# Kernel tuning notes

Measured on AMD Instinct MI355X. Metric: run time of the kernel, lower is better.

Reference implementation:

```python
import jax, jax.numpy as jnp
import numpy as np

N_EXPERTS = 8
D_IN = 1024
D_OUT = 1024
BATCH = 4096


def setup_inputs() -> dict:
    key = jax.random.key(0)
    k_x, k_w, k_b, k_a = jax.random.split(key, 4)
    xs = jax.random.normal(k_x, (BATCH, D_IN), dtype=jnp.float32)
    mxs = jnp.arange(BATCH, dtype=jnp.int32)  # opaque per-sample metadata, passed through
    actions = jax.random.randint(k_a, (BATCH,), 0, N_EXPERTS, dtype=jnp.int64)
    # Expert parameters: each submodule is Linear(D_IN -> D_OUT)
    W = jax.random.normal(k_w, (N_EXPERTS, D_OUT, D_IN), dtype=jnp.float32) / np.sqrt(D_IN)
    b = jax.random.normal(k_b, (N_EXPERTS, D_OUT), dtype=jnp.float32) * 0.01
    return {"xs": xs, "mxs": mxs, "actions": actions, "W": W, "b": b}


def reference(xs, mxs, actions, W, b):
    # Original: per-sample python loop y_i = submodule[actions[i]](x_i); cat along batch.
    # Vectorized: compute all experts densely (E small), then select per-sample row.
    y_all = jnp.einsum("bj,eij->bei", xs, W) + b[None, :, :]  # [B, E, D_OUT]
    ys = jnp.take_along_axis(y_all, actions[:, None, None].astype(jnp.int32), axis=1)
    ys = jnp.squeeze(ys, axis=1)  # [B, D_OUT]
    return (ys, mxs, actions)
```

## Files before the change

kernel.cpp:

```cpp
#include <hip/hip_runtime.h>

#define BATCH 4096
#define D_IN 1024
#define D_OUT 1024
#define N_EXPERTS 8

#define TM 64
#define TN 128
#define TK 32
#define MAX_TILES 71

#define WS_PERM    0
#define WS_STARTS  4096
#define WS_TILE_E  4112
#define WS_TILE_M  4200
#define WS_NTILES  4288

typedef __attribute__((ext_vector_type(8))) short short8;
typedef __attribute__((ext_vector_type(4))) float f32x4;

__global__ void group_kernel(const int* __restrict__ actions, int* __restrict__ ws) {
    __shared__ int cnt[N_EXPERTS];
    __shared__ int base[N_EXPERTS];
    const int t = threadIdx.x;
    if (t < N_EXPERTS) cnt[t] = 0;
    __syncthreads();
    for (int i = t; i < BATCH; i += 256) atomicAdd(&cnt[actions[i]], 1);
    __syncthreads();
    if (t == 0) {
        int s = 0, nt = 0;
        for (int e = 0; e < N_EXPERTS; ++e) {
            const int c = cnt[e];
            base[e] = s;
            ws[WS_STARTS + e] = s;
            for (int m0 = 0; m0 < c; m0 += TM) {
                ws[WS_TILE_E + nt] = e;
                ws[WS_TILE_M + nt] = m0;
                ++nt;
            }
            s += c;
            cnt[e] = 0;
        }
        ws[WS_STARTS + N_EXPERTS] = s;
        ws[WS_NTILES] = nt;
    }
    __syncthreads();
    for (int i = t; i < BATCH; i += 256) {
        const int a = actions[i];
        const int pos = base[a] + atomicAdd(&cnt[a], 1);
        ws[WS_PERM + pos] = i;
    }
}

__device__ __forceinline__ void cvt8(const float4 a, const float4 b,
                                     short8& h, short8& l) {
    float f[8] = {a.x, a.y, a.z, a.w, b.x, b.y, b.z, b.w};
#pragma unroll
    for (int i = 0; i < 8; ++i) {
        const unsigned u = __float_as_uint(f[i]);
        h[i] = (short)(u >> 16);
        const float r = f[i] - __uint_as_float(u & 0xffff0000u);
        l[i] = (short)(__float_as_uint(r) >> 16);
    }
}

__global__ __launch_bounds__(256) void moe_gemm(
    const float* __restrict__ xs, const float* __restrict__ W,
    const float* __restrict__ bias, const int* __restrict__ ws,
    float* __restrict__ out)
{
    const int tix = blockIdx.y;
    if (tix >= ws[WS_NTILES]) return;
    const int e   = ws[WS_TILE_E + tix];
    const int m0  = ws[WS_TILE_M + tix];
    const int s0  = ws[WS_STARTS + e];
    const int cnt = ws[WS_STARTS + e + 1] - s0;
    const int n0  = blockIdx.x * TN;

    __shared__ short Ahi[TM * TK];
    __shared__ short Alo[TM * TK];
    __shared__ short Bhi[TN * TK];
    __shared__ short Blo[TN * TK];
    __shared__ int   rows_s[TM];

    const int t = threadIdx.x;
    if (t < TM) {
        const int r = m0 + t;
        rows_s[t] = (r < cnt) ? ws[WS_PERM + s0 + r] : -1;
    }
    __syncthreads();

    const int lane = t & 63;
    const int wave = t >> 6;
    const int wm = (wave & 1) * 32;
    const int wn = (wave >> 1) * 64;

    const float zf = 0.f;
    f32x4 acc[2][4];
#pragma unroll
    for (int mi = 0; mi < 2; ++mi)
#pragma unroll
        for (int nj = 0; nj < 4; ++nj)
            acc[mi][nj] = (f32x4){zf, zf, zf, zf};

    const float* Wb = W + (size_t)e * (D_OUT * (size_t)D_IN) + (size_t)n0 * D_IN;

    const int j  = t & 3;
    const int rr = t >> 2;

    const int arow = rows_s[rr];
    const float* aptr = (arow >= 0) ? (xs + (size_t)arow * D_IN + j * 8) : nullptr;

    const int slotA   = (j * 16 + (rr & 15)) ^ (j << 1);
    const int aoff_st = (rr >> 4) * 512 + slotA * 8;
    const int boff0   = aoff_st;
    const int boff1   = aoff_st + 4 * 512;

    const float* qb0 = Wb + (size_t)rr * D_IN + j * 8;
    const float* qb1 = Wb + (size_t)(64 + rr) * D_IN + j * 8;

    const int rds = (lane ^ ((lane >> 4) << 1)) * 8;

    float4 ra0 = make_float4(0.f, 0.f, 0.f, 0.f), ra1 = ra0;
    if (aptr) { ra0 = *(const float4*)(aptr);     ra1 = *(const float4*)(aptr + 4); }
    float4 rb0 = *(const float4*)(qb0),           rb1 = *(const float4*)(qb0 + 4);
    float4 rb2 = *(const float4*)(qb1),           rb3 = *(const float4*)(qb1 + 4);

    for (int k0 = 0; ; ) {
        {
            short8 h, l;
            cvt8(ra0, ra1, h, l);
            *(short8*)&Ahi[aoff_st] = h;
            *(short8*)&Alo[aoff_st] = l;
            cvt8(rb0, rb1, h, l);
            *(short8*)&Bhi[boff0] = h;
            *(short8*)&Blo[boff0] = l;
            cvt8(rb2, rb3, h, l);
            *(short8*)&Bhi[boff1] = h;
            *(short8*)&Blo[boff1] = l;
        }
        __syncthreads();

        const int kn = k0 + TK;
        if (kn < D_IN) {
            if (aptr) {
                ra0 = *(const float4*)(aptr + kn);
                ra1 = *(const float4*)(aptr + kn + 4);
            }
            rb0 = *(const float4*)(qb0 + kn); rb1 = *(const float4*)(qb0 + kn + 4);
            rb2 = *(const float4*)(qb1 + kn); rb3 = *(const float4*)(qb1 + kn + 4);
        }

        short8 ah[2], al[2], bh[4], bl[4];
#pragma unroll
        for (int i2 = 0; i2 < 2; ++i2) {
            const int aoff = ((wm >> 4) + i2) * 512 + rds;
            ah[i2] = *(const short8*)&Ahi[aoff];
            al[i2] = *(const short8*)&Alo[aoff];
        }
#pragma unroll
        for (int i2 = 0; i2 < 4; ++i2) {
            const int boff = ((wn >> 4) + i2) * 512 + rds;
            bh[i2] = *(const short8*)&Bhi[boff];
            bl[i2] = *(const short8*)&Blo[boff];
        }
#pragma unroll
        for (int mi = 0; mi < 2; ++mi)
#pragma unroll
            for (int nj = 0; nj < 4; ++nj) {
                acc[mi][nj] = __builtin_amdgcn_mfma_f32_16x16x32_bf16(ah[mi], bh[nj], acc[mi][nj], 0, 0, 0);
                acc[mi][nj] = __builtin_amdgcn_mfma_f32_16x16x32_bf16(ah[mi], bl[nj], acc[mi][nj], 0, 0, 0);
                acc[mi][nj] = __builtin_amdgcn_mfma_f32_16x16x32_bf16(al[mi], bh[nj], acc[mi][nj], 0, 0, 0);
            }

        if (kn >= D_IN) break;
        k0 = kn;
        asm volatile("s_barrier" ::: "memory");
    }

    const int cl = lane & 15;
    const int qd = lane >> 4;
    float bv[4];
#pragma unroll
    for (int nj = 0; nj < 4; ++nj)
        bv[nj] = bias[e * D_OUT + n0 + wn + nj * 16 + cl];
#pragma unroll
    for (int mi = 0; mi < 2; ++mi) {
#pragma unroll
        for (int reg = 0; reg < 4; ++reg) {
            const int mloc = wm + mi * 16 + qd * 4 + reg;
            const int r = rows_s[mloc];
            if (r >= 0) {
                float* orow = out + (size_t)r * D_OUT + n0 + wn + cl;
#pragma unroll
                for (int nj = 0; nj < 4; ++nj)
                    orow[nj * 16] = acc[mi][nj][reg] + bv[nj];
            }
        }
    }
}

__global__ void meta_float_kernel(const int* __restrict__ mxs,
                                  const int* __restrict__ actions,
                                  float* __restrict__ out) {
    const int i = blockIdx.x * 256 + threadIdx.x;
    if (i < BATCH) {
        out[BATCH * D_OUT + i] = (float)mxs[i];
        out[BATCH * D_OUT + BATCH + i] = (float)actions[i];
    }
}

__global__ void meta_raw64_kernel(const int* __restrict__ mxs,
                                  const int* __restrict__ actions,
                                  float* __restrict__ out) {
    const int i = blockIdx.x * 256 + threadIdx.x;
    if (i < BATCH) {
        out[BATCH * D_OUT + i] = (float)mxs[i];
        long long* a64 = (long long*)(out + BATCH * D_OUT + BATCH);
        a64[i] = (long long)actions[i];
    }
}

extern "C" void kernel_launch(void* const* d_in, const int* in_sizes, int n_in,
                              void* d_out, int out_size, void* d_ws, size_t ws_size,
                              hipStream_t stream) {
    const float* xs      = (const float*)d_in[0];
    const int*   mxs     = (const int*)d_in[1];
    const int*   actions = (const int*)d_in[2];
    const float* W       = (const float*)d_in[3];
    const float* bias    = (const float*)d_in[4];
    float* out = (float*)d_out;
    int*   ws  = (int*)d_ws;

    group_kernel<<<1, 256, 0, stream>>>(actions, ws);

    dim3 grid(D_OUT / TN, MAX_TILES, 1);
    moe_gemm<<<grid, 256, 0, stream>>>(xs, W, bias, ws, out);

    const int metaOff = BATCH * D_OUT;
    if (out_size >= metaOff + 3 * BATCH) {
        meta_raw64_kernel<<<(BATCH + 255) / 256, 256, 0, stream>>>(mxs, actions, out);
    } else if (out_size >= metaOff + 2 * BATCH) {
        meta_float_kernel<<<(BATCH + 255) / 256, 256, 0, stream>>>(mxs, actions, out);
    }
}
```

Baseline: 145.0 us.

## Double-buffer LDS tiles and prefetch two K-steps ahead in MoE GEMM

Shared-memory A/B hi/lo tiles become double-buffered, and the K loop is restructured so global loads for step k+2 are issued while MFMAs run on one buffer and the converted data for step k+1 is written into the other. This leaves one barrier per K step instead of two, and keeps more global loads in flight to hide memory latency. In exchange it doubles LDS use, which can lower occupancy, and adds register pressure from two sets of prefetch registers.

```diff
diff --git a/kernel.cpp b/kernel.cpp
--- a/kernel.cpp
+++ b/kernel.cpp
@@ -77,10 +77,10 @@
     const int cnt = ws[WS_STARTS + e + 1] - s0;
     const int n0  = blockIdx.x * TN;
 
-    __shared__ short Ahi[TM * TK];
-    __shared__ short Alo[TM * TK];
-    __shared__ short Bhi[TN * TK];
-    __shared__ short Blo[TN * TK];
+    __shared__ short Ahi[2][TM * TK];
+    __shared__ short Alo[2][TM * TK];
+    __shared__ short Bhi[2][TN * TK];
+    __shared__ short Blo[2][TN * TK];
     __shared__ int   rows_s[TM];
 
     const int t = threadIdx.x;
@@ -121,62 +121,92 @@
 
     const int rds = (lane ^ ((lane >> 4) << 1)) * 8;
 
-    float4 ra0 = make_float4(0.f, 0.f, 0.f, 0.f), ra1 = ra0;
-    if (aptr) { ra0 = *(const float4*)(aptr);     ra1 = *(const float4*)(aptr + 4); }
-    float4 rb0 = *(const float4*)(qb0),           rb1 = *(const float4*)(qb0 + 4);
-    float4 rb2 = *(const float4*)(qb1),           rb3 = *(const float4*)(qb1 + 4);
-
-    for (int k0 = 0; ; ) {
+#define LOAD_SET(A0, A1, B0, B1, B2, B3, KOFF) do {                          \
+        const int _k = (KOFF);                                               \
+        if (aptr) {                                                          \
+            A0 = *(const float4*)(aptr + _k);                                \
+            A1 = *(const float4*)(aptr + _k + 4);                            \
+        }                                                                    \
+        B0 = *(const float4*)(qb0 + _k); B1 = *(const float4*)(qb0 + _k + 4);\
+        B2 = *(const float4*)(qb1 + _k); B3 = *(const float4*)(qb1 + _k + 4);\
+    } while (0)
+
+#define CVT_STORE_SET(A0, A1, B0, B1, B2, B3, BUF) do {                      \
+        short8 _h, _l;                                                       \
+        cvt8(A0, A1, _h, _l);                                                \
+        *(short8*)&Ahi[BUF][aoff_st] = _h; *(short8*)&Alo[BUF][aoff_st] = _l;\
+        cvt8(B0, B1, _h, _l);                                                \
+        *(short8*)&Bhi[BUF][boff0] = _h;   *(short8*)&Blo[BUF][boff0] = _l;  \
+        cvt8(B2, B3, _h, _l);                                                \
+        *(short8*)&Bhi[BUF][boff1] = _h;   *(short8*)&Blo[BUF][boff1] = _l;  \
+    } while (0)
+
+#define FRAG_MFMA(BUF) do {                                                  \
+        short8 ah[2], al[2], bh[4], bl[4];                                   \
+        _Pragma("unroll")                                                    \
+        for (int i2 = 0; i2 < 2; ++i2) {                                     \
+            const int aoff = ((wm >> 4) + i2) * 512 + rds;                   \
+            ah[i2] = *(const short8*)&Ahi[BUF][aoff];                        \
+            al[i2] = *(const short8*)&Alo[BUF][aoff];                        \
+        }                                                                    \
+        _Pragma("unroll")                                                    \
+        for (int i2 = 0; i2 < 4; ++i2) {                                     \
+            const int boff = ((wn >> 4) + i2) * 512 + rds;                   \
+            bh[i2] = *(const short8*)&Bhi[BUF][boff];                        \
+            bl[i2] = *(const short8*)&Blo[BUF][boff];                        \
+        }                                                                    \
+        _Pragma("unroll")                                                    \
+        for (int mi = 0; mi < 2; ++mi)                                       \
+            _Pragma("unroll")                                                \
+            for (int nj = 0; nj < 4; ++nj) {                                 \
+                acc[mi][nj] = __builtin_amdgcn_mfma_f32_16x16x32_bf16(ah[mi], bh[nj], acc[mi][nj], 0, 0, 0); \
+                acc[mi][nj] = __builtin_amdgcn_mfma_f32_16x16x32_bf16(ah[mi], bl[nj], acc[mi][nj], 0, 0, 0); \
+                acc[mi][nj] = __builtin_amdgcn_mfma_f32_16x16x32_bf16(al[mi], bh[nj], acc[mi][nj], 0, 0, 0); \
+            }                                                                \
+    } while (0)
+
+#define PIPE_BARRIER() asm volatile("s_waitcnt lgkmcnt(0)\n\ts_barrier" ::: "memory")
+
+    float4 ax0 = make_float4(0.f, 0.f, 0.f, 0.f), ax1 = ax0;
+    float4 bx0, bx1, bx2, bx3;
+    float4 ay0 = make_float4(0.f, 0.f, 0.f, 0.f), ay1 = ay0;
+    float4 by0, by1, by2, by3;
+
+    LOAD_SET(ax0, ax1, bx0, bx1, bx2, bx3, 0);
+    CVT_STORE_SET(ax0, ax1, bx0, bx1, bx2, bx3, 0);
+    LOAD_SET(ax0, ax1, bx0, bx1, bx2, bx3, TK);
+    PIPE_BARRIER();
+
+    int ke = 2 * TK;
+#pragma unroll 1
+    for (int i = 0; i < 15; ++i) {
         {
-            short8 h, l;
-            cvt8(ra0, ra1, h, l);
-            *(short8*)&Ahi[aoff_st] = h;
-            *(short8*)&Alo[aoff_st] = l;
-            cvt8(rb0, rb1, h, l);
-            *(short8*)&Bhi[boff0] = h;
-            *(short8*)&Blo[boff0] = l;
-            cvt8(rb2, rb3, h, l);
-            *(short8*)&Bhi[boff1] = h;
-            *(short8*)&Blo[boff1] = l;
-        }
-        __syncthreads();
-
-        const int kn = k0 + TK;
-        if (kn < D_IN) {
-            if (aptr) {
-                ra0 = *(const float4*)(aptr + kn);
-                ra1 = *(const float4*)(aptr + kn + 4);
-            }
-            rb0 = *(const float4*)(qb0 + kn); rb1 = *(const float4*)(qb0 + kn + 4);
-            rb2 = *(const float4*)(qb1 + kn); rb3 = *(const float4*)(qb1 + kn + 4);
-        }
-
-        short8 ah[2], al[2], bh[4], bl[4];
-#pragma unroll
-        for (int i2 = 0; i2 < 2; ++i2) {
-            const int aoff = ((wm >> 4) + i2) * 512 + rds;
-            ah[i2] = *(const short8*)&Ahi[aoff];
-            al[i2] = *(const short8*)&Alo[aoff];
-        }
-#pragma unroll
-        for (int i2 = 0; i2 < 4; ++i2) {
-            const int boff = ((wn >> 4) + i2) * 512 + rds;
-            bh[i2] = *(const short8*)&Bhi[boff];
-            bl[i2] = *(const short8*)&Blo[boff];
-        }
-#pragma unroll
-        for (int mi = 0; mi < 2; ++mi)
-#pragma unroll
-            for (int nj = 0; nj < 4; ++nj) {
-                acc[mi][nj] = __builtin_amdgcn_mfma_f32_16x16x32_bf16(ah[mi], bh[nj], acc[mi][nj], 0, 0, 0);
-                acc[mi][nj] = __builtin_amdgcn_mfma_f32_16x16x32_bf16(ah[mi], bl[nj], acc[mi][nj], 0, 0, 0);
-                acc[mi][nj] = __builtin_amdgcn_mfma_f32_16x16x32_bf16(al[mi], bh[nj], acc[mi][nj], 0, 0, 0);
-            }
-
-        if (kn >= D_IN) break;
-        k0 = kn;
-        asm volatile("s_barrier" ::: "memory");
-    }
+            LOAD_SET(ay0, ay1, by0, by1, by2, by3, ke);
+            FRAG_MFMA(0);
+            CVT_STORE_SET(ax0, ax1, bx0, bx1, bx2, bx3, 1);
+            PIPE_BARRIER();
+        }
+        {
+            LOAD_SET(ax0, ax1, bx0, bx1, bx2, bx3, ke + TK);
+            FRAG_MFMA(1);
+            CVT_STORE_SET(ay0, ay1, by0, by1, by2, by3, 0);
+            PIPE_BARRIER();
+        }
+        ke += 2 * TK;
+    }
+    {
+        FRAG_MFMA(0);
+        CVT_STORE_SET(ax0, ax1, bx0, bx1, bx2, bx3, 1);
+        PIPE_BARRIER();
+    }
+    {
+        FRAG_MFMA(1);
+    }
+
+#undef LOAD_SET
+#undef CVT_STORE_SET
+#undef FRAG_MFMA
+#undef PIPE_BARRIER
 
     const int cl = lane & 15;
     const int qd = lane >> 4;
```

New measurement: 141.7 us. -2.3%, faster.
